# Optimization experiments

Measured on AMD Instinct MI355X. Metric: run time of the kernel, lower is better.

## Reference

```python
import jax, jax.numpy as jnp
import numpy as np

B, L, D, H = 2, 2048, 1024, 16
d = D // H  # head dim = 64


def setup_inputs() -> dict:
    key = jax.random.key(0)
    ks = jax.random.split(key, 6)
    X = jax.random.normal(ks[0], (B, L, D), dtype=jnp.float32)
    scale = 0.02
    Wq = scale * jax.random.normal(ks[1], (D, D), dtype=jnp.float32)
    Wk = scale * jax.random.normal(ks[2], (D, D), dtype=jnp.float32)
    Wv = scale * jax.random.normal(ks[3], (D, D), dtype=jnp.float32)
    Wc = scale * jax.random.normal(ks[4], (D, D), dtype=jnp.float32)
    Ltri = scale * jax.random.normal(ks[5], (H, d, d), dtype=jnp.float32)
    return {"X": X, "Wq": Wq, "Wk": Wk, "Wv": Wv, "Wc": Wc, "Ltri": Ltri}


def reference(X, Wq, Wk, Wv, Wc, Ltri):
    # torch nn.Linear: y = x @ W.T (bias=False); dropout is identity in eval.
    Bsz, Lq, Dm = X.shape
    Q = (X @ Wq.T).reshape(Bsz, Lq, H, d)
    K = (X @ Wk.T).reshape(Bsz, Lq, H, d)
    V = (X @ Wv.T).reshape(Bsz, Lq, H, d)
    # Causal linear attention: cumulative sum of per-position K outer V.
    # W[b,l,h,:,:] = sum_{t<=l} K[b,t,h,:] outer V[b,t,h,:]
    KV = jnp.einsum('blhd,blhe->blhde', K, V)  # [B,L,H,d,d]
    KVc = jnp.cumsum(KV, axis=1)
    Y = jnp.einsum('blhd,blhde->blhe', Q, KVc)  # [B,L,H,d]
    # Learned SPD head-mixing matrix Bm = Lm @ Lm.T with Lm lower-triangular.
    mask = jnp.tril(jnp.ones((1, d, d), dtype=X.dtype))
    Lm = Ltri * mask  # [H,d,d]
    Bm = Lm @ jnp.swapaxes(Lm, -2, -1)  # [H,d,d]
    Y = jnp.einsum('hed,blhd->blhe', Bm, Y)
    Y = Y.reshape(Bsz, Lq, Dm)
    return Y @ Wc.T
```

## Files before the change

kernel.cpp:

```cpp
#include <hip/hip_runtime.h>


#define DEV static __device__ __forceinline__

typedef unsigned short u16;
typedef unsigned long long u64;
typedef __attribute__((ext_vector_type(4))) float f32x4;
typedef __attribute__((ext_vector_type(8))) short bf16x8;

DEV u16 f2bf(float f){
  union { float f; unsigned u; } v; v.f = f;
  unsigned r = v.u + 0x7FFFu + ((v.u >> 16) & 1u);
  return (u16)(r >> 16);
}

DEV void store_val(float* p, float v){ *p = v; }
DEV void store_val(u16* p, float v){ *p = f2bf(v); }

DEV void gload16(const void* g, void* l){
  __builtin_amdgcn_global_load_lds((const __attribute__((address_space(1))) void*)g,
                                   (__attribute__((address_space(3))) void*)l, 16, 0, 0);
}

__global__ __launch_bounds__(256) void prep_kernel(
    const float* __restrict__ X, u16* __restrict__ Xb,
    const float* __restrict__ Wq, u16* __restrict__ Wqb,
    const float* __restrict__ Wk, u16* __restrict__ Wkb,
    const float* __restrict__ Wv, u16* __restrict__ Wvb,
    const float* __restrict__ Wc, u16* __restrict__ Wcb,
    const float* __restrict__ Ltri, u16* __restrict__ Bmb)
{
  const int bx = blockIdx.x, tid = threadIdx.x;
  if(bx < 16){
    __shared__ float Lm[64][65];
    int h = bx;
    const float* src = Ltri + (size_t)h * 4096;
    for(int i = tid; i < 4096; i += 256){
      int e = i >> 6, k = i & 63;
      Lm[e][k] = (k <= e) ? src[i] : 0.f;
    }
    __syncthreads();
    u16* out = Bmb + (size_t)h * 4096;
    for(int i = tid; i < 4096; i += 256){
      int e = i >> 6, dk = i & 63;
      float sum = 0.f;
      int kmax = e < dk ? e : dk;
      for(int k = 0; k <= kmax; k++) sum += Lm[e][k] * Lm[dk][k];
      out[i] = f2bf(sum);
    }
  } else {
    const int n0 = 4194304, n1 = 1048576, n2 = 1048576, n3 = 1048576, n4 = 1048576;
    int total = (n0 + n1 + n2 + n3 + n4) >> 2;
    for(int i = (bx - 16) * 256 + tid; i < total; i += 2048 * 256){
      int e = i << 2;
      const float* s; u16* d;
      if(e < n0){ s = X + e; d = Xb + e; }
      else if(e < n0 + n1){ s = Wq + (e - n0); d = Wqb + (e - n0); }
      else if(e < n0 + n1 + n2){ s = Wk + (e - n0 - n1); d = Wkb + (e - n0 - n1); }
      else if(e < n0 + n1 + n2 + n3){ s = Wv + (e - n0 - n1 - n2); d = Wvb + (e - n0 - n1 - n2); }
      else { s = Wc + (e - n0 - n1 - n2 - n3); d = Wcb + (e - n0 - n1 - n2 - n3); }
      float4 v = *(const float4*)s;
      u64 pk = (u64)f2bf(v.x) | ((u64)f2bf(v.y) << 16) | ((u64)f2bf(v.z) << 32) | ((u64)f2bf(v.w) << 48);
      *(u64*)d = pk;
    }
  }
}

template<typename OutT>
DEV void gemm128_p2(const u16* __restrict__ A, const u16* __restrict__ W,
                    OutT* __restrict__ C, int bx, int by, int N, int K)
{
  __shared__ u16 L[3][8192];
  const int tid = threadIdx.x;
  const int wid = tid >> 6, lane = tid & 63;
  const int wr = wid >> 1, wc = wid & 1;
  const int lr = lane & 15, lk8 = (lane >> 4) * 8, lq = lane >> 4;
  const int srow = tid >> 2, scol = (tid & 3) * 8;
  const u16* Ag = A + (size_t)(bx * 128 + srow) * K + scol;
  const u16* Wg = W + (size_t)(by * 128 + srow) * K + scol;

  auto stagef = [&](int kt, int buf){
    const u16* a = Ag + kt * 32;
    const u16* w = Wg + kt * 32;
    gload16(a,                    &L[buf][tid * 8]);
    gload16(a + (size_t)64 * K,   &L[buf][2048 + tid * 8]);
    gload16(w,                    &L[buf][4096 + tid * 8]);
    gload16(w + (size_t)64 * K,   &L[buf][6144 + tid * 8]);
  };

  const int nt = K >> 5;
  f32x4 acc[4][4] = {};
  stagef(0, 0);
  stagef(1, 1);
  int cur = 0;
  for(int t = 0; t < nt; t++){
    if(t < nt - 1) asm volatile("s_waitcnt vmcnt(4)" ::: "memory");
    else           asm volatile("s_waitcnt vmcnt(0)" ::: "memory");
    __builtin_amdgcn_s_barrier();
    __builtin_amdgcn_sched_barrier(0);
    if(t + 2 < nt){
      int n2 = cur >= 1 ? cur - 1 : cur + 2;
      stagef(t + 2, n2);
    }
    bf16x8 af[4], bfr[4];
#pragma unroll
    for(int i = 0; i < 4; i++) af[i]  = *(const bf16x8*)&L[cur][(wr * 64 + i * 16 + lr) * 32 + lk8];
#pragma unroll
    for(int j = 0; j < 4; j++) bfr[j] = *(const bf16x8*)&L[cur][4096 + (wc * 64 + j * 16 + lr) * 32 + lk8];
#pragma unroll
    for(int i = 0; i < 4; i++)
#pragma unroll
      for(int j = 0; j < 4; j++)
        acc[i][j] = __builtin_amdgcn_mfma_f32_16x16x32_bf16(af[i], bfr[j], acc[i][j], 0, 0, 0);
    cur = cur == 2 ? 0 : cur + 1;
  }
#pragma unroll
  for(int i = 0; i < 4; i++)
#pragma unroll
    for(int j = 0; j < 4; j++)
#pragma unroll
      for(int r = 0; r < 4; r++){
        int row = bx * 128 + wr * 64 + i * 16 + lq * 4 + r;
        int col = by * 128 + wc * 64 + j * 16 + lr;
        store_val(C + (size_t)row * N + col, acc[i][j][r]);
      }
}

__global__ __launch_bounds__(256) void qkv_gemm(
    const u16* __restrict__ Xb,
    const u16* __restrict__ Wq, const u16* __restrict__ Wk, const u16* __restrict__ Wv,
    u16* __restrict__ Q, u16* __restrict__ Ko, u16* __restrict__ V,
    const u16* __restrict__ Wcb, const u16* __restrict__ Bmb, u16* __restrict__ Wcpb)
{
  if(blockIdx.y >= 24){
    int rt = blockIdx.x & 7, h = (blockIdx.x >> 3) + ((blockIdx.y - 24) << 2);
    int wid = threadIdx.x >> 6, lane = threadIdx.x & 63;
    int lr = lane & 15, lk8 = (lane >> 4) * 8, lq = lane >> 4;
    const u16* ab  = Wcb + (size_t)(rt * 128) * 1024 + h * 64;
    const u16* bm  = Bmb + (size_t)h * 4096;
    f32x4 acc[2][4] = {};
#pragma unroll
    for(int i = 0; i < 2; i++){
      int mf = wid * 2 + i;
#pragma unroll
      for(int ks = 0; ks < 2; ks++){
        bf16x8 a = *(const bf16x8*)(ab + (size_t)(mf * 16 + lr) * 1024 + ks * 32 + lk8);
#pragma unroll
        for(int nf = 0; nf < 4; nf++){
          bf16x8 bfr = *(const bf16x8*)(bm + (nf * 16 + lr) * 64 + ks * 32 + lk8);
          acc[i][nf] = __builtin_amdgcn_mfma_f32_16x16x32_bf16(a, bfr, acc[i][nf], 0, 0, 0);
        }
      }
    }
#pragma unroll
    for(int i = 0; i < 2; i++)
#pragma unroll
      for(int nf = 0; nf < 4; nf++)
#pragma unroll
        for(int r = 0; r < 4; r++){
          int row = rt * 128 + (wid * 2 + i) * 16 + lq * 4 + r;
          int col = h * 64 + nf * 16 + lr;
          Wcpb[(size_t)row * 1024 + col] = f2bf(acc[i][nf][r]);
        }
    return;
  }
  int sel = blockIdx.y >> 3, byl = blockIdx.y & 7;
  const u16* W = sel == 0 ? Wq : sel == 1 ? Wk : Wv;
  u16* C = sel == 0 ? Q : sel == 1 ? Ko : V;
  gemm128_p2<u16>(Xb, W, C, blockIdx.x, byl, 1024, 1024);
}

__global__ __launch_bounds__(256) void out_gemm(
    const u16* __restrict__ Yb, const u16* __restrict__ Wcpb, float* __restrict__ out)
{
  gemm128_p2<float>(Yb, Wcpb, out, blockIdx.x, blockIdx.y, 1024, 1024);
}

__global__ __launch_bounds__(256) void state_chunk(
    const u16* __restrict__ Kb, const u16* __restrict__ Vb,
    u16* __restrict__ VT, float* __restrict__ Sc)
{
  int bh = blockIdx.x, c = blockIdx.y;
  int b = bh >> 4, h = bh & 15;
  int tid = threadIdx.x;
  __shared__ u16 Kt[128][72];
  __shared__ u16 Vt[128][72];
  int rr = tid >> 3;
  int cc = (tid & 7) * 8;
  const u16* kg = Kb + (size_t)(b * 2048 + c * 128) * 1024 + h * 64;
  const u16* vg = Vb + (size_t)(b * 2048 + c * 128) * 1024 + h * 64;
#pragma unroll
  for(int p = 0; p < 4; p++){
    int row = rr + p * 32;
    *(int4*)&Kt[row][cc] = *(const int4*)(kg + (size_t)row * 1024 + cc);
    *(int4*)&Vt[row][cc] = *(const int4*)(vg + (size_t)row * 1024 + cc);
  }
  __syncthreads();
  {
    int d = tid >> 2, tseg = (tid & 3) * 32;
    u16* vto = VT + (size_t)bh * 64 * 2048 + (size_t)d * 2048 + c * 128 + tseg;
#pragma unroll
    for(int j = 0; j < 32; j += 8){
      u16 tmp[8] __attribute__((aligned(16)));
#pragma unroll
      for(int q = 0; q < 8; q++) tmp[q] = Vt[tseg + j + q][d];
      *(int4*)(vto + j) = *(const int4*)tmp;
    }
  }
  int wid = tid >> 6, lane = tid & 63;
  int wr = wid >> 1, wc = wid & 1;
  int lr = lane & 15, lk8 = (lane >> 4) * 8, lq = lane >> 4;
  f32x4 acc[2][2] = {};
#pragma unroll
  for(int ks = 0; ks < 4; ks++){
    bf16x8 a[2], bb[2];
#pragma unroll
    for(int i = 0; i < 2; i++){
      u16 tmp[8] __attribute__((aligned(16)));
      int e = wr * 32 + i * 16 + lr;
#pragma unroll
      for(int q = 0; q < 8; q++) tmp[q] = Vt[ks * 32 + lk8 + q][e];
      a[i] = *(const bf16x8*)tmp;
    }
#pragma unroll
    for(int j = 0; j < 2; j++){
      u16 tmp[8] __attribute__((aligned(16)));
      int dk = wc * 32 + j * 16 + lr;
#pragma unroll
      for(int q = 0; q < 8; q++) tmp[q] = Kt[ks * 32 + lk8 + q][dk];
      bb[j] = *(const bf16x8*)tmp;
    }
#pragma unroll
    for(int i = 0; i < 2; i++)
#pragma unroll
      for(int j = 0; j < 2; j++)
        acc[i][j] = __builtin_amdgcn_mfma_f32_16x16x32_bf16(a[i], bb[j], acc[i][j], 0, 0, 0);
  }
  float* out = Sc + ((size_t)bh * 16 + c) * 4096;
#pragma unroll
  for(int i = 0; i < 2; i++)
#pragma unroll
    for(int j = 0; j < 2; j++)
#pragma unroll
      for(int r = 0; r < 4; r++){
        int e = wr * 32 + i * 16 + lq * 4 + r, dk = wc * 32 + j * 16 + lr;
        out[e * 64 + dk] = acc[i][j][r];
      }
}

__global__ __launch_bounds__(256) void prefix_state(const float* __restrict__ Sc, u16* __restrict__ Scb)
{
  int bh = blockIdx.x >> 2, part = blockIdx.x & 3;
  int e4 = part * 256 + threadIdx.x;
  const float4* s = (const float4*)(Sc + (size_t)bh * 65536) + e4;
  u16* d = Scb + (size_t)bh * 65536 + e4 * 4;
  float4 run = {0.f, 0.f, 0.f, 0.f};
  for(int c = 0; c < 16; c++){
    float4 v = s[(size_t)c * 1024];
    u64 pk = (u64)f2bf(run.x) | ((u64)f2bf(run.y) << 16) | ((u64)f2bf(run.z) << 32) | ((u64)f2bf(run.w) << 48);
    *(u64*)(d + (size_t)c * 4096) = pk;
    run.x += v.x; run.y += v.y; run.z += v.z; run.w += v.w;
  }
}

__global__ __launch_bounds__(256) void chunk_attn(
    const u16* __restrict__ Q, const u16* __restrict__ Kmat,
    const u16* __restrict__ VT, const u16* __restrict__ Scb, u16* __restrict__ Y)
{
  int bh = blockIdx.x, c = blockIdx.y;
  int b = bh >> 4, h = bh & 15;
  int t = threadIdx.x, wid = t >> 6, lane = t & 63;
  int lr = lane & 15, lk8 = (lane >> 4) * 8, lq = lane >> 4;
  __shared__ u16 S[128 * 128];
  const u16* qg = Q    + (size_t)(b * 2048 + c * 128) * 1024 + h * 64;
  const u16* kg = Kmat + (size_t)(b * 2048 + c * 128) * 1024 + h * 64;
  const u16* scb = Scb + ((size_t)bh * 16 + c) * 4096;
  const u16* vt  = VT + (size_t)bh * 64 * 2048 + (size_t)c * 128;
  u16* yg = Y + (size_t)(b * 2048 + c * 128) * 1024 + h * 64;
#pragma unroll
  for(int mi = 0; mi < 2; mi++){
    int mf = wid + mi * 4;
    int Rm = mf * 16;
    if((mf & 1) == 0){
      int zr = Rm + (lane >> 2), zc = Rm + 16 + (lane & 3) * 4;
      int zoff = ((zr * 128 + zc) * 2) ^ ((zr & 7) << 4);
      *(u64*)((char*)S + zoff) = 0ULL;
    }
    bf16x8 a[2];
#pragma unroll
    for(int ks = 0; ks < 2; ks++) a[ks] = *(const bf16x8*)(qg + (size_t)(Rm + lr) * 1024 + ks * 32 + lk8);
    for(int nf = 0; nf <= mf; nf++){
      f32x4 acc = {};
#pragma unroll
      for(int ks = 0; ks < 2; ks++){
        bf16x8 bb = *(const bf16x8*)(kg + (size_t)(nf * 16 + lr) * 1024 + ks * 32 + lk8);
        acc = __builtin_amdgcn_mfma_f32_16x16x32_bf16(a[ks], bb, acc, 0, 0, 0);
      }
#pragma unroll
      for(int r = 0; r < 4; r++){
        int row = lq * 4 + r, col = lr;
        float v = acc[r];
        if(nf == mf && col > row) v = 0.f;
        int grow = Rm + row, gcol = nf * 16 + col;
        int off = ((grow * 128 + gcol) * 2) ^ ((grow & 7) << 4);
        *(u16*)((char*)S + off) = f2bf(v);
      }
    }
    f32x4 acc2[4] = {};
#pragma unroll
    for(int nf = 0; nf < 4; nf++){
#pragma unroll
      for(int ks = 0; ks < 2; ks++){
        bf16x8 bb = *(const bf16x8*)(scb + (nf * 16 + lr) * 64 + ks * 32 + lk8);
        acc2[nf] = __builtin_amdgcn_mfma_f32_16x16x32_bf16(a[ks], bb, acc2[nf], 0, 0, 0);
      }
    }
    int ksmax = mf >> 1;
    for(int ks = 0; ks <= ksmax; ks++){
      int row = Rm + lr;
      int off = ((row * 128 + ks * 32 + lk8) * 2) ^ ((row & 7) << 4);
      bf16x8 af = *(const bf16x8*)((char*)S + off);
#pragma unroll
      for(int nf = 0; nf < 4; nf++){
        bf16x8 bb = *(const bf16x8*)(vt + (size_t)(nf * 16 + lr) * 2048 + ks * 32 + lk8);
        acc2[nf] = __builtin_amdgcn_mfma_f32_16x16x32_bf16(af, bb, acc2[nf], 0, 0, 0);
      }
    }
#pragma unroll
    for(int nf = 0; nf < 4; nf++)
#pragma unroll
      for(int r = 0; r < 4; r++){
        int grow = Rm + lq * 4 + r, gcol = nf * 16 + lr;
        yg[(size_t)grow * 1024 + gcol] = f2bf(acc2[nf][r]);
      }
  }
}

extern "C" void kernel_launch(void* const* d_in, const int* in_sizes, int n_in,
                              void* d_out, int out_size, void* d_ws, size_t ws_size,
                              hipStream_t stream)
{
  const float* X    = (const float*)d_in[0];
  const float* Wq   = (const float*)d_in[1];
  const float* Wk   = (const float*)d_in[2];
  const float* Wv   = (const float*)d_in[3];
  const float* Wc   = (const float*)d_in[4];
  const float* Ltri = (const float*)d_in[5];
  float* out = (float*)d_out;

  char* ws = (char*)d_ws;
  size_t off = 0;
  auto carve = [&](size_t bytes) -> char* {
    char* p = ws + off;
    off += (bytes + 255) & ~(size_t)255;
    return p;
  };
  u16* Xb   = (u16*)carve((size_t)4194304 * 2);
  u16* Wqb  = (u16*)carve((size_t)1048576 * 2);
  u16* Wkb  = (u16*)carve((size_t)1048576 * 2);
  u16* Wvb  = (u16*)carve((size_t)1048576 * 2);
  u16* Wcb  = (u16*)carve((size_t)1048576 * 2);
  u16* Wcpb = (u16*)carve((size_t)1048576 * 2);
  u16* Bmb  = (u16*)carve((size_t)65536 * 2);
  u16* Qb   = (u16*)carve((size_t)4194304 * 2);
  u16* Kb   = (u16*)carve((size_t)4194304 * 2);
  u16* Vb   = (u16*)carve((size_t)4194304 * 2);
  u16* VT   = (u16*)carve((size_t)4194304 * 2);
  float* Sc = (float*)carve((size_t)2097152 * 4);
  u16* Scb  = (u16*)carve((size_t)2097152 * 2);
  u16* Yb   = (u16*)carve((size_t)4194304 * 2);
  (void)in_sizes; (void)n_in; (void)out_size; (void)ws_size;

  prep_kernel<<<2064, 256, 0, stream>>>(X, Xb, Wq, Wqb, Wk, Wkb, Wv, Wvb, Wc, Wcb, Ltri, Bmb);
  qkv_gemm<<<dim3(32, 28), 256, 0, stream>>>(Xb, Wqb, Wkb, Wvb, Qb, Kb, Vb, Wcb, Bmb, Wcpb);
  state_chunk<<<dim3(32, 16), 256, 0, stream>>>(Kb, Vb, VT, Sc);
  prefix_state<<<128, 256, 0, stream>>>(Sc, Scb);
  chunk_attn<<<dim3(32, 16), 256, 0, stream>>>(Qb, Kb, VT, Scb, Yb);
  out_gemm<<<dim3(32, 8), 256, 0, stream>>>(Yb, Wcpb, out);
}
```

Measured before the change: 106.8 us.

## Use BK=64 double-buffered GEMM staging with XOR-swizzled LDS layout

Restructures the shared GEMM mainloop from a triple-buffered K=32 pipeline to a double-buffered K=64 pipeline, halving the number of barrier iterations. An XOR swizzle on the 16-byte chunk index is applied when loading from global to LDS and when reading from LDS, to avoid bank conflicts on the 128-byte rows. The cost is a second barrier per iteration and only one tile of prefetch depth, so less global-load latency can be hidden.

Result: no change. 106.0 us (-0.7%).

```diff
diff --git a/kernel.cpp b/kernel.cpp
--- a/kernel.cpp
+++ b/kernel.cpp
@@ -70,49 +70,64 @@
 DEV void gemm128_p2(const u16* __restrict__ A, const u16* __restrict__ W,
                     OutT* __restrict__ C, int bx, int by, int N, int K)
 {
-  __shared__ u16 L[3][8192];
+  __shared__ u16 L[2][16384];
   const int tid = threadIdx.x;
   const int wid = tid >> 6, lane = tid & 63;
   const int wr = wid >> 1, wc = wid & 1;
-  const int lr = lane & 15, lk8 = (lane >> 4) * 8, lq = lane >> 4;
-  const int srow = tid >> 2, scol = (tid & 3) * 8;
-  const u16* Ag = A + (size_t)(bx * 128 + srow) * K + scol;
-  const u16* Wg = W + (size_t)(by * 128 + srow) * K + scol;
+  const int lr = lane & 15, lq = lane >> 4, lk8 = lq * 8;
+  const int srow = tid >> 3;
+  const int schunk = tid & 7;
+  const u16* Ag = A + (size_t)(bx * 128) * K;
+  const u16* Wg = W + (size_t)(by * 128) * K;
 
   auto stagef = [&](int kt, int buf){
-    const u16* a = Ag + kt * 32;
-    const u16* w = Wg + kt * 32;
-    gload16(a,                    &L[buf][tid * 8]);
-    gload16(a + (size_t)64 * K,   &L[buf][2048 + tid * 8]);
-    gload16(w,                    &L[buf][4096 + tid * 8]);
-    gload16(w + (size_t)64 * K,   &L[buf][6144 + tid * 8]);
+#pragma unroll
+    for(int p = 0; p < 4; p++){
+      int row = p * 32 + srow;
+      int sc = ((schunk ^ (row & 7)) * 8);
+      gload16(Ag + (size_t)row * K + kt * 64 + sc, &L[buf][p * 2048 + tid * 8]);
+    }
+#pragma unroll
+    for(int p = 0; p < 4; p++){
+      int row = p * 32 + srow;
+      int sc = ((schunk ^ (row & 7)) * 8);
+      gload16(Wg + (size_t)row * K + kt * 64 + sc, &L[buf][8192 + p * 2048 + tid * 8]);
+    }
   };
 
-  const int nt = K >> 5;
+  const int nt = K >> 6;
   f32x4 acc[4][4] = {};
   stagef(0, 0);
-  stagef(1, 1);
-  int cur = 0;
   for(int t = 0; t < nt; t++){
-    if(t < nt - 1) asm volatile("s_waitcnt vmcnt(4)" ::: "memory");
-    else           asm volatile("s_waitcnt vmcnt(0)" ::: "memory");
+    if(t + 1 < nt){
+      stagef(t + 1, (t + 1) & 1);
+      asm volatile("s_waitcnt vmcnt(8)" ::: "memory");
+    } else {
+      asm volatile("s_waitcnt vmcnt(0)" ::: "memory");
+    }
     __builtin_amdgcn_s_barrier();
     __builtin_amdgcn_sched_barrier(0);
-    if(t + 2 < nt){
-      int n2 = cur >= 1 ? cur - 1 : cur + 2;
-      stagef(t + 2, n2);
-    }
-    bf16x8 af[4], bfr[4];
-#pragma unroll
-    for(int i = 0; i < 4; i++) af[i]  = *(const bf16x8*)&L[cur][(wr * 64 + i * 16 + lr) * 32 + lk8];
-#pragma unroll
-    for(int j = 0; j < 4; j++) bfr[j] = *(const bf16x8*)&L[cur][4096 + (wc * 64 + j * 16 + lr) * 32 + lk8];
-#pragma unroll
-    for(int i = 0; i < 4; i++)
-#pragma unroll
-      for(int j = 0; j < 4; j++)
-        acc[i][j] = __builtin_amdgcn_mfma_f32_16x16x32_bf16(af[i], bfr[j], acc[i][j], 0, 0, 0);
-    cur = cur == 2 ? 0 : cur + 1;
+    const u16* Lb = L[t & 1];
+#pragma unroll
+    for(int ks = 0; ks < 2; ks++){
+      bf16x8 af[4], bfr[4];
+#pragma unroll
+      for(int i = 0; i < 4; i++){
+        int row = wr * 64 + i * 16 + lr;
+        af[i] = *(const bf16x8*)&Lb[row * 64 + (((ks * 4 + lq) ^ (row & 7)) * 8)];
+      }
+#pragma unroll
+      for(int j = 0; j < 4; j++){
+        int row = wc * 64 + j * 16 + lr;
+        bfr[j] = *(const bf16x8*)&Lb[8192 + row * 64 + (((ks * 4 + lq) ^ (row & 7)) * 8)];
+      }
+#pragma unroll
+      for(int i = 0; i < 4; i++)
+#pragma unroll
+        for(int j = 0; j < 4; j++)
+          acc[i][j] = __builtin_amdgcn_mfma_f32_16x16x32_bf16(af[i], bfr[j], acc[i][j], 0, 0, 0);
+    }
+    __builtin_amdgcn_s_barrier();
   }
 #pragma unroll
   for(int i = 0; i < 4; i++)
```
